# Performance work log

Hardware: AMD Instinct MI355X
Metric: run time of the kernel (lower is better)

The kernel has to match this reference:

```python
import jax, jax.numpy as jnp
import numpy as np

EPS = 1e-08
SURROGATE_SCALE = 10.0  # SuperSpike surrogate slope

@jax.custom_vjp
def spike_fn(v):
    # Heaviside forward, SuperSpike surrogate gradient backward
    return (v > 0).astype(v.dtype)

def _spike_fwd(v):
    return spike_fn(v), v

def _spike_bwd(v, g):
    return (g / (1.0 + SURROGATE_SCALE * jnp.abs(v)) ** 2,)

spike_fn.defvjp(_spike_fwd, _spike_bwd)


def setup_inputs() -> dict:
    key = jax.random.key(0)
    k1, k2, k3, k4 = jax.random.split(key, 4)
    B, C, T = 64, 256, 2048
    x = jax.random.normal(k1, (B, C, T), dtype=jnp.float32)
    conv_weight = jax.random.normal(k2, (C, C, 3), dtype=jnp.float32) * 0.05
    beta = jnp.clip(0.7 + 0.01 * jax.random.normal(k3, (1,), dtype=jnp.float32), 0.0, 1.0)
    b = jnp.clip(1.0 + 0.01 * jax.random.normal(k4, (C,), dtype=jnp.float32), 0.0, None)
    return {"x": x, "conv_weight": conv_weight, "beta": beta, "b": b}


def reference(x, conv_weight, beta, b):
    # x: (B, C, T); LIF recurrence over T with scaled threshold/reset
    norm = (conv_weight ** 2).sum((1, 2))          # (C,)
    inv_norm = 1.0 / (norm + EPS)                   # (C,)
    B, C, T = x.shape
    xt = jnp.transpose(x, (2, 0, 1))                # (T, B, C)

    def step(carry, inp):
        mem, spk = carry
        rst = spk * (b * norm)                      # einsum ab,b,b->ab
        mem = (mem - rst) * beta + inp * (1.0 - beta)
        mthr = mem * inv_norm - b
        spk = spike_fn(mthr)
        return (mem, spk), spk

    init = (jnp.zeros((B, C), x.dtype), jnp.zeros((B, C), x.dtype))
    _, spk_rec = jax.lax.scan(step, init, xt)       # (T, B, C)
    return jnp.transpose(spk_rec, (1, 2, 0))        # (B, C, T), flatten_output=False
```

## Files before the change

### kernel.cpp

```cpp
#include <hip/hip_runtime.h>

#define C_DIM 256
#define T_DIM 2048
#define NROWS (64 * C_DIM)
#define NV 16
#define NCHUNK (T_DIM / (NV * 4))

__device__ __forceinline__ float sqrn(float v) { return __fmul_rn(v, v); }

__global__ __launch_bounds__(64) void norm_kernel(const float* __restrict__ w,
                                                  const float* __restrict__ b,
                                                  float* __restrict__ bn,
                                                  float* __restrict__ ninv) {
    const int c = blockIdx.x;
    const int k = threadIdx.x;
    __shared__ float q[8];
    if (k < 8) {
        const float* a = w + c * 768 + k * 96;
        float r0 = sqrn(a[0]), r1 = sqrn(a[1]), r2 = sqrn(a[2]), r3 = sqrn(a[3]);
        float r4 = sqrn(a[4]), r5 = sqrn(a[5]), r6 = sqrn(a[6]), r7 = sqrn(a[7]);
        #pragma unroll
        for (int i = 8; i < 96; i += 8) {
            r0 = __fadd_rn(r0, sqrn(a[i + 0]));
            r1 = __fadd_rn(r1, sqrn(a[i + 1]));
            r2 = __fadd_rn(r2, sqrn(a[i + 2]));
            r3 = __fadd_rn(r3, sqrn(a[i + 3]));
            r4 = __fadd_rn(r4, sqrn(a[i + 4]));
            r5 = __fadd_rn(r5, sqrn(a[i + 5]));
            r6 = __fadd_rn(r6, sqrn(a[i + 6]));
            r7 = __fadd_rn(r7, sqrn(a[i + 7]));
        }
        q[k] = __fadd_rn(__fadd_rn(__fadd_rn(r0, r1), __fadd_rn(r2, r3)),
                         __fadd_rn(__fadd_rn(r4, r5), __fadd_rn(r6, r7)));
    }
    __syncthreads();
    if (k == 0) {
        float s = __fadd_rn(__fadd_rn(__fadd_rn(q[0], q[1]), __fadd_rn(q[2], q[3])),
                            __fadd_rn(__fadd_rn(q[4], q[5]), __fadd_rn(q[6], q[7])));
        bn[c]   = __fmul_rn(b[c], s);
        ninv[c] = 1.0f / __fadd_rn(s, 1e-8f);
    }
}

__device__ __forceinline__ float lif_step(float xv, float& mem, float& spk,
                                          float bnc, float beta, float omb,
                                          float nic, float bc) {
    float rst  = __fmul_rn(spk, bnc);
    mem        = __fadd_rn(__fmul_rn(__fsub_rn(mem, rst), beta),
                           __fmul_rn(xv, omb));
    float mthr = __fsub_rn(__fmul_rn(mem, nic), bc);
    spk        = (mthr > 0.0f) ? 1.0f : 0.0f;
    return spk;
}

__global__ __launch_bounds__(64, 1) void lif_kernel(const float* __restrict__ x,
                                                    const float* __restrict__ beta_p,
                                                    const float* __restrict__ b,
                                                    const float* __restrict__ bn,
                                                    const float* __restrict__ ninv,
                                                    float* __restrict__ out) {
    const int row = blockIdx.x * 64 + threadIdx.x;
    const int c   = row & (C_DIM - 1);

    const float beta = beta_p[0];
    const float omb  = __fsub_rn(1.0f, beta);
    const float bnc  = bn[c];
    const float nic  = ninv[c];
    const float bc   = b[c];

    const float4* xp = (const float4*)(x + (size_t)row * T_DIM);
    float4*       op = (float4*)(out + (size_t)row * T_DIM);

    float4 bufA[NV], bufB[NV];
    #pragma unroll
    for (int i = 0; i < NV; ++i) bufA[i] = xp[i];

    float mem = 0.0f, spk = 0.0f;

    #pragma unroll 1
    for (int ch = 0; ch < NCHUNK; ch += 2) {
        #pragma unroll
        for (int i = 0; i < NV; ++i) bufB[i] = xp[(ch + 1) * NV + i];
        #pragma unroll
        for (int i = 0; i < NV; ++i) {
            float4 v = bufA[i], o;
            o.x = lif_step(v.x, mem, spk, bnc, beta, omb, nic, bc);
            o.y = lif_step(v.y, mem, spk, bnc, beta, omb, nic, bc);
            o.z = lif_step(v.z, mem, spk, bnc, beta, omb, nic, bc);
            o.w = lif_step(v.w, mem, spk, bnc, beta, omb, nic, bc);
            op[ch * NV + i] = o;
        }
        if (ch + 2 < NCHUNK) {
            #pragma unroll
            for (int i = 0; i < NV; ++i) bufA[i] = xp[(ch + 2) * NV + i];
        }
        #pragma unroll
        for (int i = 0; i < NV; ++i) {
            float4 v = bufB[i], o;
            o.x = lif_step(v.x, mem, spk, bnc, beta, omb, nic, bc);
            o.y = lif_step(v.y, mem, spk, bnc, beta, omb, nic, bc);
            o.z = lif_step(v.z, mem, spk, bnc, beta, omb, nic, bc);
            o.w = lif_step(v.w, mem, spk, bnc, beta, omb, nic, bc);
            op[(ch + 1) * NV + i] = o;
        }
    }
}

extern "C" void kernel_launch(void* const* d_in, const int* in_sizes, int n_in,
                              void* d_out, int out_size, void* d_ws, size_t ws_size,
                              hipStream_t stream) {
    const float* x    = (const float*)d_in[0];
    const float* w    = (const float*)d_in[1];
    const float* beta = (const float*)d_in[2];
    const float* b    = (const float*)d_in[3];
    float* out  = (float*)d_out;
    float* bn   = (float*)d_ws;
    float* ninv = bn + C_DIM;

    norm_kernel<<<C_DIM, 64, 0, stream>>>(w, b, bn, ninv);
    lif_kernel<<<NROWS / 64, 64, 0, stream>>>(x, beta, b, bn, ninv, out);
}
```

Baseline: 278.7 us.

## Stage x tiles through LDS with async global_load_lds and coalesced stores

After: 284.8 us. 2.2% more time.

```diff
diff --git a/kernel.cpp b/kernel.cpp
--- a/kernel.cpp
+++ b/kernel.cpp
@@ -2,9 +2,12 @@
 
 #define C_DIM 256
 #define T_DIM 2048
-#define NROWS (64 * C_DIM)
-#define NV 16
-#define NCHUNK (T_DIM / (NV * 4))
+#define B_DIM 64
+#define NROWS (B_DIM * C_DIM)
+#define RPB 64
+#define TW 256
+#define NT (T_DIM / TW)
+#define RSTRIDE 260
 
 __device__ __forceinline__ float sqrn(float v) { return __fmul_rn(v, v); }
 
@@ -53,14 +56,24 @@
     return spk;
 }
 
+#define WAITCNT_VM0    0x0F70
+#define WAITCNT_VM62   0xCF7E
+#define WAITCNT_LGKM0  0xC07F
+
+#define LDS_PTR(p) ((__attribute__((address_space(3))) void*)(p))
+#define GLB_PTR(p) ((const __attribute__((address_space(1))) void*)(p))
+
 __global__ __launch_bounds__(64, 1) void lif_kernel(const float* __restrict__ x,
                                                     const float* __restrict__ beta_p,
                                                     const float* __restrict__ b,
                                                     const float* __restrict__ bn,
                                                     const float* __restrict__ ninv,
                                                     float* __restrict__ out) {
-    const int row = blockIdx.x * 64 + threadIdx.x;
-    const int c   = row & (C_DIM - 1);
+    __shared__ __align__(16) float lds[2][RPB * RSTRIDE];
+
+    const int lane = threadIdx.x;
+    const int row0 = blockIdx.x * RPB;
+    const int c    = (row0 + lane) & (C_DIM - 1);
 
     const float beta = beta_p[0];
     const float omb  = __fsub_rn(1.0f, beta);
@@ -68,40 +81,52 @@
     const float nic  = ninv[c];
     const float bc   = b[c];
 
-    const float4* xp = (const float4*)(x + (size_t)row * T_DIM);
-    float4*       op = (float4*)(out + (size_t)row * T_DIM);
+    const float* xbase = x + (size_t)row0 * T_DIM + lane * 4;
+    float*       obase = out + (size_t)row0 * T_DIM + lane * 4;
 
-    float4 bufA[NV], bufB[NV];
     #pragma unroll
-    for (int i = 0; i < NV; ++i) bufA[i] = xp[i];
+    for (int r = 0; r < RPB; ++r) {
+        __builtin_amdgcn_global_load_lds(GLB_PTR(xbase + (size_t)r * T_DIM),
+                                         LDS_PTR(&lds[0][r * RSTRIDE]), 16, 0, 0);
+    }
 
     float mem = 0.0f, spk = 0.0f;
 
     #pragma unroll 1
-    for (int ch = 0; ch < NCHUNK; ch += 2) {
-        #pragma unroll
-        for (int i = 0; i < NV; ++i) bufB[i] = xp[(ch + 1) * NV + i];
-        #pragma unroll
-        for (int i = 0; i < NV; ++i) {
-            float4 v = bufA[i], o;
+    for (int k = 0; k < NT; ++k) {
+        if (k == 0) __builtin_amdgcn_s_waitcnt(WAITCNT_VM0);
+        else        __builtin_amdgcn_s_waitcnt(WAITCNT_VM62);
+
+        if (k + 1 < NT) {
+            const float* xt = xbase + (size_t)(k + 1) * TW;
+            #pragma unroll
+            for (int r = 0; r < RPB; ++r) {
+                __builtin_amdgcn_global_load_lds(GLB_PTR(xt + (size_t)r * T_DIM),
+                                                 LDS_PTR(&lds[(k + 1) & 1][r * RSTRIDE]),
+                                                 16, 0, 0);
+            }
+        }
+
+        float* buf = &lds[k & 1][0];
+        float* myrow = buf + lane * RSTRIDE;
+        #pragma unroll 4
+        for (int g = 0; g < TW / 4; ++g) {
+            float4 v = *(const float4*)(myrow + 4 * g);
+            float4 o;
             o.x = lif_step(v.x, mem, spk, bnc, beta, omb, nic, bc);
             o.y = lif_step(v.y, mem, spk, bnc, beta, omb, nic, bc);
             o.z = lif_step(v.z, mem, spk, bnc, beta, omb, nic, bc);
             o.w = lif_step(v.w, mem, spk, bnc, beta, omb, nic, bc);
-            op[ch * NV + i] = o;
+            *(float4*)(myrow + 4 * g) = o;
         }
-        if (ch + 2 < NCHUNK) {
-            #pragma unroll
-            for (int i = 0; i < NV; ++i) bufA[i] = xp[(ch + 2) * NV + i];
-        }
+
+        __builtin_amdgcn_s_waitcnt(WAITCNT_LGKM0);
+
+        float* ot = obase + (size_t)k * TW;
         #pragma unroll
-        for (int i = 0; i < NV; ++i) {
-            float4 v = bufB[i], o;
-            o.x = lif_step(v.x, mem, spk, bnc, beta, omb, nic, bc);
-            o.y = lif_step(v.y, mem, spk, bnc, beta, omb, nic, bc);
-            o.z = lif_step(v.z, mem, spk, bnc, beta, omb, nic, bc);
-            o.w = lif_step(v.w, mem, spk, bnc, beta, omb, nic, bc);
-            op[(ch + 1) * NV + i] = o;
+        for (int r = 0; r < RPB; ++r) {
+            float4 v = *(const float4*)(buf + r * RSTRIDE + 4 * lane);
+            *(float4*)(ot + (size_t)r * T_DIM) = v;
         }
     }
 }
@@ -118,5 +143,5 @@
     float* ninv = bn + C_DIM;
 
     norm_kernel<<<C_DIM, 64, 0, stream>>>(w, b, bn, ninv);
-    lif_kernel<<<NROWS / 64, 64, 0, stream>>>(x, beta, b, bn, ninv, out);
+    lif_kernel<<<NROWS / RPB, 64, 0, stream>>>(x, beta, b, bn, ninv, out);
 }
```
